# Performance work log

Hardware: AMD Instinct MI355X
Metric: run time of the kernel (lower is better)

Reference implementation:

```python
import jax, jax.numpy as jnp
import numpy as np

B, T, N, E = 16, 30, 2048, 32768
F_IN, HID, TEMP, NCLS = 8, 64, 128, 2
EPS = 1e-5  # BatchNorm eps (eval mode, running stats)


def setup_inputs() -> dict:
    key = jax.random.key(0)
    ks = jax.random.split(key, 26)
    def gl(k, shape, fan_in):
        return (jax.random.normal(k, shape, jnp.float32) / np.sqrt(fan_in)).astype(jnp.float32)
    inp = {}
    inp["x"] = jax.random.normal(ks[0], (B, T, N, F_IN), jnp.float32)
    inp["edge_index"] = jax.random.randint(ks[1], (B, T, 2, E), 0, N)
    inp["edge_weight"] = jax.random.uniform(ks[2], (B, T, E), jnp.float32)
    inp["node_ids"] = jax.random.randint(ks[3], (B, T, N), 0, 1000000)
    # GCN layer 1 and 2 (PyG GCNConv: x @ W then normalized aggregation, + bias)
    inp["W1"] = gl(ks[4], (F_IN, HID), F_IN); inp["b1"] = jnp.zeros((HID,), jnp.float32)
    inp["W2"] = gl(ks[5], (HID, HID), HID);   inp["b2"] = jnp.zeros((HID,), jnp.float32)
    # BatchNorm1d params (eval mode with running stats)
    inp["g1"] = jnp.ones((HID,), jnp.float32); inp["be1"] = jnp.zeros((HID,), jnp.float32)
    inp["m1"] = 0.1 * jax.random.normal(ks[6], (HID,), jnp.float32)
    inp["v1"] = jnp.ones((HID,), jnp.float32) + 0.1 * jax.random.uniform(ks[7], (HID,))
    inp["g2"] = jnp.ones((HID,), jnp.float32); inp["be2"] = jnp.zeros((HID,), jnp.float32)
    inp["m2"] = 0.1 * jax.random.normal(ks[8], (HID,), jnp.float32)
    inp["v2"] = jnp.ones((HID,), jnp.float32) + 0.1 * jax.random.uniform(ks[9], (HID,))
    # GRU (PyTorch layout: W_ih [3*TEMP, HID], W_hh [3*TEMP, TEMP])
    inp["Wih"] = gl(ks[10], (3 * TEMP, HID), HID)
    inp["Whh"] = gl(ks[11], (3 * TEMP, TEMP), TEMP)
    inp["bih"] = jnp.zeros((3 * TEMP,), jnp.float32)
    inp["bhh"] = jnp.zeros((3 * TEMP,), jnp.float32)
    # Classifier MLP: TEMP -> TEMP//2 -> NCLS
    inp["Wc1"] = gl(ks[12], (TEMP, TEMP // 2), TEMP); inp["bc1"] = jnp.zeros((TEMP // 2,), jnp.float32)
    inp["Wc2"] = gl(ks[13], (TEMP // 2, NCLS), TEMP // 2); inp["bc2"] = jnp.zeros((NCLS,), jnp.float32)
    return inp


def _gcn(h, src, dst, ew, W, b):
    # PyG GCNConv with self-loops (weight 1) and symmetric normalization.
    hw = h @ W                                     # [N, out]
    deg = jnp.ones((N,), hw.dtype).at[dst].add(ew)  # in-degree incl. self-loop
    dinv = jnp.where(deg > 0, jax.lax.rsqrt(deg), 0.0)
    norm = dinv[src] * ew * dinv[dst]               # [E]
    agg = jnp.zeros_like(hw).at[dst].add(norm[:, None] * hw[src])
    agg = agg + (dinv * dinv)[:, None] * hw         # self-loop contribution
    return agg + b


def _frame(x, ei, ew, nid, W1, b1, g1, be1, m1, v1, W2, b2, g2, be2, m2, v2):
    # node_ids identity alignment: sort rows of x by node_ids
    x = x[jnp.argsort(nid)]
    src, dst = ei[0], ei[1]
    h = _gcn(x, src, dst, ew, W1, b1)
    h = (h - m1) * jax.lax.rsqrt(v1 + EPS) * g1 + be1  # BN eval
    h = jax.nn.relu(h)
    h = _gcn(h, src, dst, ew, W2, b2)
    h = (h - m2) * jax.lax.rsqrt(v2 + EPS) * g2 + be2
    h = jax.nn.relu(h)
    return h.mean(axis=0)  # frame embedding [HID]


def _forward(x, edge_weight, W1, b1, g1, be1, m1, v1, W2, b2, g2, be2, m2, v2,
             Wih, Whh, bih, bhh, Wc1, bc1, Wc2, bc2, edge_index, node_ids):
    G = B * T
    frames = jax.vmap(
        lambda xf, eif, ewf, nidf: _frame(xf, eif, ewf, nidf, W1, b1, g1, be1,
                                          m1, v1, W2, b2, g2, be2, m2, v2)
    )(x.reshape(G, N, F_IN), edge_index.reshape(G, 2, E),
      edge_weight.reshape(G, E), node_ids.reshape(G, N))
    H = frames.reshape(B, T, HID).transpose(1, 0, 2)  # [T, B, HID]

    def gru_step(h, xt):
        gi = xt @ Wih.T + bih
        gh = h @ Whh.T + bhh
        ir, iz, inn = jnp.split(gi, 3, axis=-1)
        hr, hz, hn = jnp.split(gh, 3, axis=-1)
        r = jax.nn.sigmoid(ir + hr)
        z = jax.nn.sigmoid(iz + hz)
        n = jnp.tanh(inn + r * hn)
        return (1.0 - z) * n + z * h, None

    h0 = jnp.zeros((B, TEMP), H.dtype)
    h_final, _ = jax.lax.scan(gru_step, h0, H)
    hidden = jax.nn.relu(h_final @ Wc1 + bc1)
    return hidden @ Wc2 + bc2  # [B, NCLS]


def reference(x, edge_index, edge_weight, node_ids, W1, b1, W2, b2, g1, be1, m1, v1,
              g2, be2, m2, v2, Wih, Whh, bih, bhh, Wc1, bc1, Wc2, bc2):
    return _forward(x, edge_weight, W1, b1, g1, be1, m1, v1, W2, b2, g2, be2, m2, v2,
                    Wih, Whh, bih, bhh, Wc1, bc1, Wc2, bc2, edge_index, node_ids)
```

## Files before the change

kernel.cpp:

```cpp
#include <hip/hip_runtime.h>
#include <hip/hip_fp16.h>
#include <stdint.h>

#define B_   16
#define T_   30
#define NF   480
#define NN   2048
#define EE   32768
#define EPS  1e-5f

typedef unsigned int u32;
typedef unsigned short u16;
typedef __attribute__((ext_vector_type(8))) short short8;
typedef __attribute__((ext_vector_type(4))) float f32x4;

__device__ __forceinline__ u16 f2bf(float f) {
  u32 u = __float_as_uint(f);
  u32 r = u + 0x7FFFu + ((u >> 16) & 1u);
  return (u16)(r >> 16);
}
__device__ __forceinline__ u32 pack2bf(float a, float b) {
  return (u32)f2bf(a) | ((u32)f2bf(b) << 16);
}
__device__ __forceinline__ u16 f2h(float f) { return __half_as_ushort(__float2half(f)); }
__device__ __forceinline__ float h2f(u16 h) { return __half2float(__ushort_as_half(h)); }
__device__ __forceinline__ u32 pack2h(float a, float b) {
  return (u32)f2h(a) | ((u32)f2h(b) << 16);
}

#define AGG_FRAME_U16 131072
#define STASH_DINV_U16 4096

#define KM_KEYS 0
#define KM_DEG  8192
#define KM_CNT  16384
#define KM_PR   24576
#define KM_HIST 32768
#define KM_CUM  33792
#define KM_CUR  34816
#define KM_LDS  35840

__global__ __launch_bounds__(1024) void kMeta(
    const int* __restrict__ ei, const float* __restrict__ ew, const int* __restrict__ nid,
    u32* __restrict__ metaR, float* __restrict__ dv2R, u32* __restrict__ offG,
    u16* __restrict__ aggStash,
    const float* __restrict__ W2, const float* __restrict__ b2,
    const float* __restrict__ g2, const float* __restrict__ be2,
    const float* __restrict__ m2, const float* __restrict__ v2,
    const float* __restrict__ W1, const float* __restrict__ b1,
    const float* __restrict__ g1, const float* __restrict__ be1,
    const float* __restrict__ m1, const float* __restrict__ v1,
    u16* __restrict__ W2bT, float* __restrict__ scG, float* __restrict__ tcG,
    float* __restrict__ W1f, float* __restrict__ t1f)
{
  extern __shared__ unsigned char smem[];
  const int g = blockIdx.x, t = threadIdx.x;
  const int*   eig  = ei  + (size_t)g * 2 * EE;
  const float* ewg  = ew  + (size_t)g * EE;
  const int*   nidg = nid + (size_t)g * NN;

  u32*  keys = (u32*)(smem + KM_KEYS);
  float* deg = (float*)(smem + KM_DEG);
  u32*  cnt  = (u32*)(smem + KM_CNT);
  u32*  pr   = (u32*)(smem + KM_PR);
  u32*  hist = (u32*)(smem + KM_HIST);
  u32*  cum  = (u32*)(smem + KM_CUM);
  u32*  cur  = (u32*)(smem + KM_CUR);

  u32*  npG  = (u32*)(aggStash + (size_t)g * AGG_FRAME_U16);
  u16*  dvG  = aggStash + (size_t)g * AGG_FRAME_U16 + STASH_DINV_U16;

  keys[t]        = ((u32)nidg[t] << 11) | (u32)t;
  keys[t + 1024] = ((u32)nidg[t + 1024] << 11) | (u32)(t + 1024);
  deg[t] = 1.0f; deg[t + 1024] = 1.0f;
  cnt[t] = 0u; cnt[t + 1024] = 0u;
  __syncthreads();

  for (int k = 2; k <= NN; k <<= 1) {
    for (int j = k >> 1; j > 0; j >>= 1) {
      int i = ((t & ~(j - 1)) << 1) | (t & (j - 1));
      int l = i | j;
      u32 x = keys[i], y = keys[l];
      bool up = ((i & k) == 0);
      if ((x > y) == up) { keys[i] = y; keys[l] = x; }
      __syncthreads();
    }
  }
  pr[2*t]   = (keys[2*t]   & 2047u) << 16;
  pr[2*t+1] = (keys[2*t+1] & 2047u) << 16;

  for (int e = t; e < EE; e += 1024) {
    int d = eig[EE + e];
    atomicAdd(&deg[d], ewg[e]);
    atomicAdd(&cnt[d], 1u);
  }
  __syncthreads();
  {
    float d0 = rsqrtf(deg[2*t]), d1 = rsqrtf(deg[2*t+1]);
    dvG[2*t] = f2h(d0); dvG[2*t+1] = f2h(d1);
    deg[2*t] = d0; deg[2*t+1] = d1;
  }

  if (t < 256) hist[t] = 0u;
  __syncthreads();
  for (int i = t; i < NN; i += 1024) {
    u32 L = cnt[i];
    atomicAdd(&hist[L < 255u ? L : 255u], 1u);
  }
  __syncthreads();
  if (t < 256) cum[t] = hist[t];
  __syncthreads();
  for (int o = 1; o < 256; o <<= 1) {
    u32 v = 0u;
    if (t < 256 && t >= o) v = cum[t - o];
    __syncthreads();
    if (t < 256) cum[t] += v;
    __syncthreads();
  }
  if (t < 256) cur[t] = (u32)NN - cum[t];
  __syncthreads();
  if (t < 256) hist[t] = cur[t];
  __syncthreads();
  for (int o = 1; o < 256; o <<= 1) {
    u32 v = 0u;
    if (t < 256 && t >= o) v = hist[t - o];
    __syncthreads();
    if (t < 256) hist[t] += v;
    __syncthreads();
  }
  if (t < 256) offG[(size_t)g * 256 + t] = hist[t] - cur[t];
  __syncthreads();

  for (int i = t; i < NN; i += 1024) {
    u32 L = cnt[i];
    u32 b = L < 255u ? L : 255u;
    u32 r = atomicAdd(&cur[b], 1u);
    pr[i] |= r;
    metaR[(size_t)g * NN + r] = (pr[i] & 0xFFFF0000u) | (L & 0xFFFFu);
    float dv = deg[i];
    dv2R[(size_t)g * NN + r] = dv * dv;
  }
  __syncthreads();
  npG[2*t]   = pr[2*t];
  npG[2*t+1] = pr[2*t+1];

  if (g == 0) {
    for (int i = t; i < 4096; i += 1024) {
      int f = i >> 6, k = i & 63;
      W2bT[i] = f2bf(W2[k * 64 + f]);
    }
    if (t < 512) {
      int f = t & 63;
      float sc = g1[f] * rsqrtf(v1[f] + EPS);
      W1f[t] = W1[t] * sc;
    }
    if (t < 64) {
      float sc2 = g2[t] * rsqrtf(v2[t] + EPS);
      scG[t] = sc2;
      tcG[t] = (b2[t] - m2[t]) * sc2 + be2[t];
      float sc1 = g1[t] * rsqrtf(v1[t] + EPS);
      t1f[t] = (b1[t] - m1[t]) * sc1 + be1[t];
    }
  }
}

#define KS_REC  0
#define KS_CNT  131072
#define KS_PR   139264
#define KS_DINV 147456
#define KS_OFF  151552
#define KS_LDS  152576

__global__ __launch_bounds__(1024) void kScatter(
    const int* __restrict__ ei, const float* __restrict__ ew,
    const u32* __restrict__ offG, const u16* __restrict__ aggStash,
    u32* __restrict__ recG)
{
  extern __shared__ unsigned char smem[];
  const int g = blockIdx.x, t = threadIdx.x;
  const int*   eig = ei + (size_t)g * 2 * EE;
  const float* ewg = ew + (size_t)g * EE;

  u32* rec   = (u32*)(smem + KS_REC);
  u32* cnt   = (u32*)(smem + KS_CNT);
  u32* prL   = (u32*)(smem + KS_PR);
  u16* dinvL = (u16*)(smem + KS_DINV);
  u32* off   = (u32*)(smem + KS_OFF);

  const u32* npG = (const u32*)(aggStash + (size_t)g * AGG_FRAME_U16);
  const u16* dvG = aggStash + (size_t)g * AGG_FRAME_U16 + STASH_DINV_U16;

  prL[2*t] = npG[2*t]; prL[2*t+1] = npG[2*t+1];
  dinvL[2*t] = dvG[2*t]; dinvL[2*t+1] = dvG[2*t+1];
  cnt[t] = 0u; cnt[t + 1024] = 0u;
  if (t < 256) off[t] = offG[(size_t)g * 256 + t];
  __syncthreads();

  for (int e = t; e < EE; e += 1024) {
    int s = eig[e], d = eig[EE + e];
    float nrm = h2f(dinvL[s]) * ewg[e] * h2f(dinvL[d]);
    u32 k = atomicAdd(&cnt[d], 1u);
    u32 pos = off[k] + (prL[d] & 0xFFFFu);
    rec[pos] = (prL[s] & 0xFFFF0000u) | (u32)f2h(nrm);
  }
  __syncthreads();

  uint4* rg = (uint4*)(recG + (size_t)g * EE);
  const uint4* rl = (const uint4*)rec;
  for (int i = t; i < EE / 4; i += 1024) rg[i] = rl[i];
}

#define KF_H1   0
#define KF_W1   65536
#define KF_T1   67584
#define KF_OFF  67840
#define KF_LDS  68864

__global__ __launch_bounds__(1024) void kFuse(
    const float* __restrict__ x, const u32* __restrict__ recG,
    const u32* __restrict__ metaR, const float* __restrict__ dv2R,
    const u32* __restrict__ offG,
    const float* __restrict__ W1f, const float* __restrict__ t1f,
    u16* __restrict__ aggOut)
{
  extern __shared__ unsigned char smem[];
  u16*  h1   = (u16*)smem;
  float* W1s = (float*)(smem + KF_W1);
  float* t1s = (float*)(smem + KF_T1);
  u32*  offL = (u32*)(smem + KF_OFF);
  const int g = blockIdx.x, t = threadIdx.x;
  const u32* recf = recG + (size_t)g * EE;

  {
    const float4* xg = (const float4*)(x + (size_t)g * NN * 8);
    for (int i = t; i < NN * 2; i += 1024) ((float4*)smem)[i] = xg[i];
  }
  if (t < 512) W1s[t] = W1f[t];
  if (t < 64) t1s[t] = t1f[t];
  if (t >= 512 && t < 768) offL[t - 512] = offG[(size_t)g * 256 + (t - 512)];

  u32 origA[2], lenA[2]; float dvA[2];
  #pragma unroll
  for (int it = 0; it < 2; ++it) {
    u32 r = (u32)(it * 1024 + t);
    u32 m = metaR[(size_t)g * NN + r];
    origA[it] = m >> 16; lenA[it] = m & 0xFFFFu;
    dvA[it] = dv2R[(size_t)g * NN + r];
  }
  __syncthreads();

  float agg[2][8];
#define P1(RC) { u32 rc_ = (RC); u32 s_ = rc_ >> 16; \
    float nm_ = h2f((u16)(rc_ & 0xFFFFu)); \
    const float4* xp_ = (const float4*)(smem + (size_t)s_ * 32); \
    float4 a_ = xp_[0], b_ = xp_[1]; \
    ac0 += nm_*a_.x; ac1 += nm_*a_.y; ac2 += nm_*a_.z; ac3 += nm_*a_.w; \
    ac4 += nm_*b_.x; ac5 += nm_*b_.y; ac6 += nm_*b_.z; ac7 += nm_*b_.w; }
  #pragma unroll
  for (int it = 0; it < 2; ++it) {
    u32 r = (u32)(it * 1024 + t);
    float ac0=0,ac1=0,ac2=0,ac3=0,ac4=0,ac5=0,ac6=0,ac7=0;
    int len = (int)lenA[it];
    int j = 0;
    for (; j + 4 <= len; j += 4) {
      u32 o0 = offL[j], o1 = offL[j+1], o2 = offL[j+2], o3 = offL[j+3];
      u32 q0 = recf[o0 + r], q1 = recf[o1 + r], q2 = recf[o2 + r], q3 = recf[o3 + r];
      P1(q0) P1(q1) P1(q2) P1(q3)
    }
    for (; j < len; ++j) { P1(recf[offL[j] + r]) }
    {
      const float4* xd = (const float4*)(smem + (size_t)origA[it] * 32);
      float4 a = xd[0], b = xd[1];
      float dv = dvA[it];
      ac0 += dv*a.x; ac1 += dv*a.y; ac2 += dv*a.z; ac3 += dv*a.w;
      ac4 += dv*b.x; ac5 += dv*b.y; ac6 += dv*b.z; ac7 += dv*b.w;
    }
    agg[it][0]=ac0; agg[it][1]=ac1; agg[it][2]=ac2; agg[it][3]=ac3;
    agg[it][4]=ac4; agg[it][5]=ac5; agg[it][6]=ac6; agg[it][7]=ac7;
  }
#undef P1

  for (int p = 0; p < 4; ++p) {
    __syncthreads();

    #pragma unroll
    for (int it = 0; it < 2; ++it) {
      float z[16];
      #pragma unroll
      for (int f = 0; f < 16; ++f) z[f] = t1s[p * 16 + f];
      #pragma unroll
      for (int k = 0; k < 8; ++k) {
        float fk = agg[it][k];
        const float4* wr = (const float4*)(W1s + k * 64 + p * 16);
        #pragma unroll
        for (int q = 0; q < 4; ++q) {
          float4 w = wr[q];
          z[4*q]   += fk * w.x; z[4*q+1] += fk * w.y;
          z[4*q+2] += fk * w.z; z[4*q+3] += fk * w.w;
        }
      }
      u32 orig = origA[it];
      u32 sw = (orig >> 2) & 1u;
      uint4* hp = (uint4*)(h1 + (size_t)orig * 16);
      #pragma unroll
      for (int u = 0; u < 2; ++u) {
        int b = u * 8;
        uint4 v = make_uint4(
          pack2h(fmaxf(z[b],   0.f), fmaxf(z[b+1], 0.f)),
          pack2h(fmaxf(z[b+2], 0.f), fmaxf(z[b+3], 0.f)),
          pack2h(fmaxf(z[b+4], 0.f), fmaxf(z[b+5], 0.f)),
          pack2h(fmaxf(z[b+6], 0.f), fmaxf(z[b+7], 0.f)));
        hp[u ^ sw] = v;
      }
    }
    __syncthreads();

#define ROWACC(SRC, NM, OP) { u32 s_ = (SRC); float nm_ = (NM); \
    u32 sw_ = (s_ >> 2) & 1u; \
    const uint4* rp_ = (const uint4*)(h1 + (size_t)s_ * 16); \
    _Pragma("unroll") \
    for (int u = 0; u < 2; ++u) { \
      uint4 w_ = rp_[u ^ sw_]; \
      int b_ = u * 8; \
      acc[b_+0] OP nm_ * h2f((u16)(w_.x & 0xFFFFu)); \
      acc[b_+1] OP nm_ * h2f((u16)(w_.x >> 16)); \
      acc[b_+2] OP nm_ * h2f((u16)(w_.y & 0xFFFFu)); \
      acc[b_+3] OP nm_ * h2f((u16)(w_.y >> 16)); \
      acc[b_+4] OP nm_ * h2f((u16)(w_.z & 0xFFFFu)); \
      acc[b_+5] OP nm_ * h2f((u16)(w_.z >> 16)); \
      acc[b_+6] OP nm_ * h2f((u16)(w_.w & 0xFFFFu)); \
      acc[b_+7] OP nm_ * h2f((u16)(w_.w >> 16)); \
    } }

    for (int it = 0; it < 2; ++it) {
      u32 r = (u32)(it * 1024 + t);
      float acc[16];
      ROWACC(origA[it], dvA[it], =)
      int len = (int)lenA[it];
      if (len > 0) {
        u32 qn = recf[offL[0] + r];
        int j = 0;
        for (; j < len - 1; ++j) {
          u32 q = qn;
          qn = recf[offL[j + 1] + r];
          ROWACC(q >> 16, h2f((u16)(q & 0xFFFFu)), +=)
        }
        ROWACC(qn >> 16, h2f((u16)(qn & 0xFFFFu)), +=)
      }
      #pragma unroll
      for (int u = 0; u < 2; ++u) {
        int b = u * 8;
        uint4 o = make_uint4(
          pack2bf(acc[b],   acc[b+1]), pack2bf(acc[b+2], acc[b+3]),
          pack2bf(acc[b+4], acc[b+5]), pack2bf(acc[b+6], acc[b+7]));
        *((uint4*)aggOut + ((size_t)(g * 8 + p * 2 + u)) * NN + r) = o;
      }
    }
#undef ROWACC
  }
}

__global__ __launch_bounds__(512) void kB(
    const u16* __restrict__ agg, const u16* __restrict__ W2bT,
    const float* __restrict__ scG, const float* __restrict__ tcG,
    float* __restrict__ frames)
{
  __shared__ u16 W2s[4096];
  __shared__ float part[8][64];
  const int g = blockIdx.x, tid = threadIdx.x;
  const int l = tid & 63, w = tid >> 6;
  const int lc = l & 15, lg = l >> 4;

  ((uint4*)W2s)[tid] = ((const uint4*)W2bT)[tid];
  __syncthreads();

  short8 bfr[4][2];
  float scv[4], tcv[4];
  #pragma unroll
  for (int ct = 0; ct < 4; ++ct) {
    #pragma unroll
    for (int kt = 0; kt < 2; ++kt)
      bfr[ct][kt] = *(const short8*)(W2s + (ct * 16 + lc) * 64 + kt * 32 + lg * 8);
    scv[ct] = scG[ct * 16 + lc];
    tcv[ct] = tcG[ct * 16 + lc];
  }

  const u16* base = agg + (size_t)g * (8 * NN * 8);
  float fs0 = 0.f, fs1 = 0.f, fs2 = 0.f, fs3 = 0.f;

  for (int rti = 0; rti < 16; ++rti) {
    int arow = (w * 16 + rti) * 16 + lc;
    short8 a0 = *(const short8*)(base + ((size_t)(0 * 4 + lg) * NN + arow) * 8);
    short8 a1 = *(const short8*)(base + ((size_t)(1 * 4 + lg) * NN + arow) * 8);
#define CTILE(CT, FS) { \
    f32x4 acc = {0.f, 0.f, 0.f, 0.f}; \
    acc = __builtin_amdgcn_mfma_f32_16x16x32_bf16(a0, bfr[CT][0], acc, 0, 0, 0); \
    acc = __builtin_amdgcn_mfma_f32_16x16x32_bf16(a1, bfr[CT][1], acc, 0, 0, 0); \
    float s_ = fmaxf(acc[0] * scv[CT] + tcv[CT], 0.f) \
             + fmaxf(acc[1] * scv[CT] + tcv[CT], 0.f) \
             + fmaxf(acc[2] * scv[CT] + tcv[CT], 0.f) \
             + fmaxf(acc[3] * scv[CT] + tcv[CT], 0.f); \
    s_ += __shfl_xor(s_, 16); \
    s_ += __shfl_xor(s_, 32); \
    FS += s_; }
    CTILE(0, fs0) CTILE(1, fs1) CTILE(2, fs2) CTILE(3, fs3)
#undef CTILE
  }
  if (l < 16) {
    part[w][ 0 + l] = fs0;
    part[w][16 + l] = fs1;
    part[w][32 + l] = fs2;
    part[w][48 + l] = fs3;
  }
  __syncthreads();
  if (tid < 64) {
    float s = 0.f;
    #pragma unroll
    for (int q = 0; q < 8; ++q) s += part[q][tid];
    frames[g * 64 + tid] = s * (1.0f / 2048.0f);
  }
}

__global__ __launch_bounds__(384, 2) void kC(
    const float* __restrict__ frames,
    const float* __restrict__ Wih, const float* __restrict__ Whh,
    const float* __restrict__ bih, const float* __restrict__ bhh,
    const float* __restrict__ Wc1, const float* __restrict__ bc1,
    const float* __restrict__ Wc2, const float* __restrict__ bc2,
    float* __restrict__ out)
{
  const int b = blockIdx.x;
  const int j = threadIdx.x;
  __shared__ float xt[64], h[128], GI[384], GH[384], hid[64];
  float wih[64], whh[128];
  const float4* wi4 = (const float4*)(Wih + (size_t)j * 64);
  #pragma unroll
  for (int q = 0; q < 16; ++q) { float4 v = wi4[q]; wih[4*q]=v.x; wih[4*q+1]=v.y; wih[4*q+2]=v.z; wih[4*q+3]=v.w; }
  const float4* wh4 = (const float4*)(Whh + (size_t)j * 128);
  #pragma unroll
  for (int q = 0; q < 32; ++q) { float4 v = wh4[q]; whh[4*q]=v.x; whh[4*q+1]=v.y; whh[4*q+2]=v.z; whh[4*q+3]=v.w; }
  float bi = bih[j], bh = bhh[j];
  if (j < 128) h[j] = 0.f;
  __syncthreads();
  for (int t = 0; t < T_; ++t) {
    if (j < 64) xt[j] = frames[((size_t)b * T_ + t) * 64 + j];
    __syncthreads();
    float gi = bi, gh = bh;
    #pragma unroll
    for (int k = 0; k < 64; ++k) gi += xt[k] * wih[k];
    #pragma unroll
    for (int k = 0; k < 128; ++k) gh += h[k] * whh[k];
    GI[j] = gi; GH[j] = gh;
    __syncthreads();
    if (j < 128) {
      float r = 1.f / (1.f + __expf(-(GI[j] + GH[j])));
      float z = 1.f / (1.f + __expf(-(GI[128 + j] + GH[128 + j])));
      float n = tanhf(GI[256 + j] + r * GH[256 + j]);
      h[j] = (1.f - z) * n + z * h[j];
    }
    __syncthreads();
  }
  if (j < 64) {
    float a = bc1[j];
    #pragma unroll 4
    for (int k = 0; k < 128; ++k) a += h[k] * Wc1[k * 64 + j];
    hid[j] = fmaxf(a, 0.f);
  }
  __syncthreads();
  if (j < 2) {
    float o = bc2[j];
    #pragma unroll
    for (int k = 0; k < 64; ++k) o += hid[k] * Wc2[k * 2 + j];
    out[b * 2 + j] = o;
  }
}

extern "C" void kernel_launch(void* const* d_in, const int* in_sizes, int n_in,
                              void* d_out, int out_size, void* d_ws, size_t ws_size,
                              hipStream_t stream) {
  const float* x   = (const float*)d_in[0];
  const int*   ei  = (const int*)d_in[1];
  const float* ew  = (const float*)d_in[2];
  const int*   nid = (const int*)d_in[3];
  const float* W1  = (const float*)d_in[4];
  const float* b1  = (const float*)d_in[5];
  const float* W2  = (const float*)d_in[6];
  const float* b2  = (const float*)d_in[7];
  const float* g1  = (const float*)d_in[8];
  const float* be1 = (const float*)d_in[9];
  const float* m1  = (const float*)d_in[10];
  const float* v1  = (const float*)d_in[11];
  const float* g2  = (const float*)d_in[12];
  const float* be2 = (const float*)d_in[13];
  const float* m2  = (const float*)d_in[14];
  const float* v2  = (const float*)d_in[15];
  const float* Wih = (const float*)d_in[16];
  const float* Whh = (const float*)d_in[17];
  const float* bih = (const float*)d_in[18];
  const float* bhh = (const float*)d_in[19];
  const float* Wc1 = (const float*)d_in[20];
  const float* bc1 = (const float*)d_in[21];
  const float* Wc2 = (const float*)d_in[22];
  const float* bc2 = (const float*)d_in[23];
  float* out = (float*)d_out;

  const size_t REC_OFF   = 0;
  const size_t PL_OFF    = 62914560;
  const size_t META_OFF  = 188743680;
  const size_t DV2_OFF   = 192675840;
  const size_t OFF_OFF   = 196608000;
  const size_t PREP_OFF  = 197099520;
  const size_t FR_OFF    = 197110528;
  if (ws_size < (size_t)197233408) return;

  u32*   rec   = (u32*)((char*)d_ws + REC_OFF);
  u16*   agg2  = (u16*)((char*)d_ws + PL_OFF);
  u32*   metaR = (u32*)((char*)d_ws + META_OFF);
  float* dv2R  = (float*)((char*)d_ws + DV2_OFF);
  u32*   offG  = (u32*)((char*)d_ws + OFF_OFF);
  u16*   W2bT  = (u16*)((char*)d_ws + PREP_OFF);
  float* scG   = (float*)((char*)d_ws + PREP_OFF + 8192);
  float* tcG   = (float*)((char*)d_ws + PREP_OFF + 8448);
  float* W1f   = (float*)((char*)d_ws + PREP_OFF + 8704);
  float* t1f   = (float*)((char*)d_ws + PREP_OFF + 10752);
  float* frm   = (float*)((char*)d_ws + FR_OFF);

  hipFuncSetAttribute((const void*)kMeta,    hipFuncAttributeMaxDynamicSharedMemorySize, KM_LDS);
  hipFuncSetAttribute((const void*)kScatter, hipFuncAttributeMaxDynamicSharedMemorySize, KS_LDS);
  hipFuncSetAttribute((const void*)kFuse,    hipFuncAttributeMaxDynamicSharedMemorySize, KF_LDS);

  kMeta<<<NF, 1024, KM_LDS, stream>>>(ei, ew, nid, metaR, dv2R, offG, agg2,
                                      W2, b2, g2, be2, m2, v2,
                                      W1, b1, g1, be1, m1, v1,
                                      W2bT, scG, tcG, W1f, t1f);
  kScatter<<<NF, 1024, KS_LDS, stream>>>(ei, ew, offG, agg2, rec);
  kFuse<<<NF, 1024, KF_LDS, stream>>>(x, rec, metaR, dv2R, offG, W1f, t1f, agg2);
  kB<<<NF, 512, 0, stream>>>(agg2, W2bT, scG, tcG, frm);
  kC<<<B_, 384, 0, stream>>>(frm, Wih, Whh, bih, bhh, Wc1, bc1, Wc2, bc2, out);
}
```

Before: 425.1 us.

## Replace bitonic sort of node keys with bucket counting sort plus in-bucket ranking

The per-frame bitonic sort over 2048 keys, which needs about 66 barrier-separated passes, is replaced by a histogram on the top key bits, a prefix scan, a scatter into buckets and a rank-by-comparison within each bucket. The aim is to cut the barrier count and shared-memory traffic in the metadata kernel. It adds more shared memory and atomics. Ranking cost grows with bucket occupancy, and the shared-memory layout is reorganised so deg and cnt alias the scratch buffers.

```diff
diff --git a/kernel.cpp b/kernel.cpp
--- a/kernel.cpp
+++ b/kernel.cpp
@@ -31,14 +31,15 @@
 #define AGG_FRAME_U16 131072
 #define STASH_DINV_U16 4096
 
-#define KM_KEYS 0
-#define KM_DEG  8192
-#define KM_CNT  16384
-#define KM_PR   24576
-#define KM_HIST 32768
-#define KM_CUM  33792
-#define KM_CUR  34816
-#define KM_LDS  35840
+#define KM_A    0
+#define KM_B    8192
+#define KM_C    16384
+#define KM_D    24576
+#define KM_PR   32768
+#define KM_HIST 40960
+#define KM_CUM  41984
+#define KM_CUR  43008
+#define KM_LDS  44032
 
 __global__ __launch_bounds__(1024) void kMeta(
     const int* __restrict__ ei, const float* __restrict__ ew, const int* __restrict__ nid,
@@ -59,9 +60,12 @@
   const float* ewg  = ew  + (size_t)g * EE;
   const int*   nidg = nid + (size_t)g * NN;
 
-  u32*  keys = (u32*)(smem + KM_KEYS);
-  float* deg = (float*)(smem + KM_DEG);
-  u32*  cnt  = (u32*)(smem + KM_CNT);
+  u32*  A    = (u32*)(smem + KM_A);
+  u32*  Btmp = (u32*)(smem + KM_B);
+  u32*  C    = (u32*)(smem + KM_C);
+  u32*  D    = (u32*)(smem + KM_D);
+  float* deg = (float*)(smem + KM_C);
+  u32*  cnt  = (u32*)(smem + KM_D);
   u32*  pr   = (u32*)(smem + KM_PR);
   u32*  hist = (u32*)(smem + KM_HIST);
   u32*  cum  = (u32*)(smem + KM_CUM);
@@ -70,24 +74,49 @@
   u32*  npG  = (u32*)(aggStash + (size_t)g * AGG_FRAME_U16);
   u16*  dvG  = aggStash + (size_t)g * AGG_FRAME_U16 + STASH_DINV_U16;
 
-  keys[t]        = ((u32)nidg[t] << 11) | (u32)t;
-  keys[t + 1024] = ((u32)nidg[t + 1024] << 11) | (u32)(t + 1024);
+  u32 k0 = ((u32)nidg[t] << 11) | (u32)t;
+  u32 k1 = ((u32)nidg[t + 1024] << 11) | (u32)(t + 1024);
+  D[t] = 0u; D[t + 1024] = 0u;
+  __syncthreads();
+  atomicAdd(&D[k0 >> 20], 1u);
+  atomicAdd(&D[k1 >> 20], 1u);
+  __syncthreads();
+  u32 c0 = D[2*t], c1 = D[2*t+1];
+  Btmp[t] = c0 + c1;
+  __syncthreads();
+  for (int o = 1; o < 1024; o <<= 1) {
+    u32 v = (t >= o) ? Btmp[t - o] : 0u;
+    __syncthreads();
+    Btmp[t] += v;
+    __syncthreads();
+  }
+  {
+    u32 base = (t == 0) ? 0u : Btmp[t - 1];
+    C[2*t] = base; C[2*t+1] = base + c0;
+  }
+  D[t] = 0u; D[t + 1024] = 0u;
+  __syncthreads();
+  {
+    u32 b0 = k0 >> 20, b1 = k1 >> 20;
+    Btmp[C[b0] + atomicAdd(&D[b0], 1u)] = k0;
+    Btmp[C[b1] + atomicAdd(&D[b1], 1u)] = k1;
+  }
+  __syncthreads();
+  for (int p = t; p < NN; p += 1024) {
+    u32 k = Btmp[p];
+    u32 b = k >> 20;
+    u32 s = C[b], e = s + D[b];
+    u32 r = 0;
+    for (u32 q = s; q < e; ++q) r += (Btmp[q] < k) ? 1u : 0u;
+    A[s + r] = k;
+  }
+  __syncthreads();
+
+  pr[2*t]   = (A[2*t]   & 2047u) << 16;
+  pr[2*t+1] = (A[2*t+1] & 2047u) << 16;
   deg[t] = 1.0f; deg[t + 1024] = 1.0f;
   cnt[t] = 0u; cnt[t + 1024] = 0u;
   __syncthreads();
-
-  for (int k = 2; k <= NN; k <<= 1) {
-    for (int j = k >> 1; j > 0; j >>= 1) {
-      int i = ((t & ~(j - 1)) << 1) | (t & (j - 1));
-      int l = i | j;
-      u32 x = keys[i], y = keys[l];
-      bool up = ((i & k) == 0);
-      if ((x > y) == up) { keys[i] = y; keys[l] = x; }
-      __syncthreads();
-    }
-  }
-  pr[2*t]   = (keys[2*t]   & 2047u) << 16;
-  pr[2*t+1] = (keys[2*t+1] & 2047u) << 16;
 
   for (int e = t; e < EE; e += 1024) {
     int d = eig[EE + e];
```

After: 419.6 us. Within noise of the previous version (-1.3%).
